# Performance work log

Measured on AMD Instinct MI355X. Metric: run time of the kernel, lower is better.

## Reference

```python
import jax, jax.numpy as jnp
import numpy as np

D_MODEL = 256
NHEAD = 8
NLAYERS = 4
DFF = 1024
PATCH = 8
INPUT = 32
C = 2
DATA_DIM = C * PATCH * PATCH  # 128
P = (INPUT // PATCH) ** 2     # 16
NEG = -1.0e6                  # _neg_large_for_dtype(float32)
EPS = 1e-5


def _ln(x, w, b):
    m = x.mean(-1, keepdims=True)
    v = ((x - m) ** 2).mean(-1, keepdims=True)
    return (x - m) / jnp.sqrt(v + EPS) * w + b


def _forward(img_baseline, acq_dts_float, nan_token, pad_embed, emb_w, emb_b, spatial_pos,
             t_w1, t_b1, t_w2, t_b2, t_w3, t_b3,
             in_proj_w, in_proj_b, out_proj_w, out_proj_b,
             lin1_w, lin1_b, lin2_w, lin2_b, norm1_w, norm1_b, norm2_w, norm2_b,
             mean_w1, mean_b1, mean_w2, mean_b2, lv_w1, lv_b1, lv_w2, lv_b2):
    B, T, Cc, Hh, Ww = img_baseline.shape
    p = PATCH
    gh, gw = Hh // p, Ww // p
    L = T * P
    frame_pad = jnp.all(img_baseline == -9999.0, axis=(2, 3, 4))  # (B,T)
    nan_pix = jnp.isnan(img_baseline)
    token = jnp.clip(nan_token, -10.0, 10.0).reshape(1, 1, Cc, 1, 1)
    x = jnp.clip(jnp.where(nan_pix, token, img_baseline), -10.0, 10.0)

    def patchify(a):  # b t c (h ph)(w pw) -> b t (h w) (c ph pw)
        return a.reshape(B, T, Cc, gh, p, gw, p).transpose(0, 1, 3, 5, 2, 4, 6).reshape(B, T, P, Cc * p * p)

    xp = patchify(x)
    seq_nan = patchify(nan_pix).all(-1).reshape(B, L)
    seq_pad = jnp.broadcast_to(frame_pad[:, :, None], (B, T, P)).reshape(B, L)

    # temporal MLP embedding
    t_in = jnp.where(jnp.isnan(acq_dts_float), 0.0, acq_dts_float)[..., None]  # (B,T,1)
    h = jax.nn.relu(t_in @ t_w1.T + t_b1)
    h = jax.nn.relu(h @ t_w2.T + t_b2)
    temb = h @ t_w3.T + t_b3  # (B,T,D)

    z = xp @ emb_w.T + emb_b + spatial_pos + temb[:, :, None, :]  # (B,T,P,D)
    z = z.reshape(B, L, D_MODEL)
    z = jnp.where(seq_pad[..., None], pad_embed, z)  # masked_scatter of pad_embed

    # additive attention mask: rows with NaN/pad patches are fully masked except diagonal
    masked_rows = seq_nan | seq_pad
    mask = jnp.broadcast_to(jnp.where(masked_rows[:, :, None], NEG, 0.0), (B, L, L))
    eye = jnp.eye(L, dtype=bool)
    mask = jnp.where(eye[None, :, :] & masked_rows[:, :, None], 0.0, mask)
    # key_padding_mask merged additively on key columns
    mask = mask + jnp.where(seq_pad[:, None, :], NEG, 0.0)
    mask = mask[:, None, :, :]  # (B,1,L,L), shared across heads

    dh = D_MODEL // NHEAD
    scale = 1.0 / np.sqrt(dh).astype(np.float32)
    for l in range(NLAYERS):
        qkv = z @ in_proj_w[l].T + in_proj_b[l]
        q, k, v = jnp.split(qkv, 3, axis=-1)
        q = q.reshape(B, L, NHEAD, dh).transpose(0, 2, 1, 3)
        k = k.reshape(B, L, NHEAD, dh).transpose(0, 2, 1, 3)
        v = v.reshape(B, L, NHEAD, dh).transpose(0, 2, 1, 3)
        scores = jnp.einsum('bhqd,bhkd->bhqk', q, k) * scale + mask
        attn = jax.nn.softmax(scores, axis=-1)
        o = jnp.einsum('bhqk,bhkd->bhqd', attn, v).transpose(0, 2, 1, 3).reshape(B, L, D_MODEL)
        o = o @ out_proj_w[l].T + out_proj_b[l]
        z = _ln(z + o, norm1_w[l], norm1_b[l])
        ff = jax.nn.relu(z @ lin1_w[l].T + lin1_b[l]) @ lin2_w[l].T + lin2_b[l]
        z = _ln(z + ff, norm2_w[l], norm2_b[l])

    mean = jnp.clip(jax.nn.relu(z @ mean_w1.T + mean_b1) @ mean_w2.T + mean_b2, -10.0, 10.0)
    logvar = jnp.clip(jax.nn.relu(z @ lv_w1.T + lv_b1) @ lv_w2.T + lv_b2, -10.0, 5.0)

    def unpatch(a):  # b t (h w)(c ph pw) -> b t c (h ph)(w pw)
        return a.reshape(B, T, gh, gw, Cc, p, p).transpose(0, 1, 4, 2, 5, 3, 6).reshape(B, T, Cc, Hh, Ww)

    mean = unpatch(mean.reshape(B, T, P, DATA_DIM))
    logvar = unpatch(logvar.reshape(B, T, P, DATA_DIM))
    return mean[:, -1], logvar[:, -1]


def setup_inputs() -> dict:
    key = jax.random.key(0)
    ks = iter(jax.random.split(key, 48))

    def rn(shape, scale=0.02):
        return jax.random.normal(next(ks), shape, dtype=jnp.float32) * scale

    B, T = 4, 64
    z = lambda s: jnp.zeros(s, jnp.float32)
    return {
        'img_baseline': jax.random.normal(next(ks), (B, T, C, INPUT, INPUT), dtype=jnp.float32),
        'acq_dts_float': jax.random.uniform(next(ks), (B, T), dtype=jnp.float32) * 3000.0,
        'nan_token': rn((C,)),
        'pad_embed': rn((1, 1, D_MODEL)),
        'emb_w': rn((D_MODEL, DATA_DIM)),
        'emb_b': z((D_MODEL,)),
        'spatial_pos': rn((1, 1, P, D_MODEL)),
        't_w1': rn((64, 1)), 't_b1': z((64,)),
        't_w2': rn((128, 64)), 't_b2': z((128,)),
        't_w3': rn((D_MODEL, 128)), 't_b3': z((D_MODEL,)),
        'in_proj_w': rn((NLAYERS, 3 * D_MODEL, D_MODEL)),
        'in_proj_b': z((NLAYERS, 3 * D_MODEL)),
        'out_proj_w': rn((NLAYERS, D_MODEL, D_MODEL)),
        'out_proj_b': z((NLAYERS, D_MODEL)),
        'lin1_w': rn((NLAYERS, DFF, D_MODEL)), 'lin1_b': z((NLAYERS, DFF)),
        'lin2_w': rn((NLAYERS, D_MODEL, DFF)), 'lin2_b': z((NLAYERS, D_MODEL)),
        'norm1_w': jnp.ones((NLAYERS, D_MODEL), jnp.float32), 'norm1_b': z((NLAYERS, D_MODEL)),
        'norm2_w': jnp.ones((NLAYERS, D_MODEL), jnp.float32), 'norm2_b': z((NLAYERS, D_MODEL)),
        'mean_w1': rn((DFF, D_MODEL)), 'mean_b1': z((DFF,)),
        'mean_w2': rn((DATA_DIM, DFF)), 'mean_b2': z((DATA_DIM,)),
        'lv_w1': rn((DFF, D_MODEL)), 'lv_b1': z((DFF,)),
        'lv_w2': rn((DATA_DIM, DFF)), 'lv_b2': z((DATA_DIM,)),
    }


def reference(img_baseline, acq_dts_float, nan_token, pad_embed, emb_w, emb_b, spatial_pos,
              t_w1, t_b1, t_w2, t_b2, t_w3, t_b3,
              in_proj_w, in_proj_b, out_proj_w, out_proj_b,
              lin1_w, lin1_b, lin2_w, lin2_b, norm1_w, norm1_b, norm2_w, norm2_b,
              mean_w1, mean_b1, mean_w2, mean_b2, lv_w1, lv_b1, lv_w2, lv_b2):
    return _forward(img_baseline, acq_dts_float, nan_token, pad_embed, emb_w, emb_b, spatial_pos,
                    t_w1, t_b1, t_w2, t_b2, t_w3, t_b3,
                    in_proj_w, in_proj_b, out_proj_w, out_proj_b,
                    lin1_w, lin1_b, lin2_w, lin2_b, norm1_w, norm1_b, norm2_w, norm2_b,
                    mean_w1, mean_b1, mean_w2, mean_b2, lv_w1, lv_b1, lv_w2, lv_b2)
```

## Files before the change

### kernel.cpp

```cpp
#include <hip/hip_runtime.h>
#include <hip/hip_bf16.h>

#define D_MODEL 256
#define NHEAD 8
#define DH 32
#define NLAYERS 4
#define DFF 1024
#define CC 2
#define DATA_DIM 128
#define PP 16
#define TT 64
#define BB 4
#define LL 1024
#define NEGV -1000000.0f

typedef __bf16 bf16_t;
typedef __bf16 bf16x8 __attribute__((ext_vector_type(8)));
typedef __bf16 bf16x4 __attribute__((ext_vector_type(4)));
typedef float v4f __attribute__((ext_vector_type(4)));

__device__ __forceinline__ bool my_isnan(float v) {
    unsigned u = __float_as_uint(v);
    return (u & 0x7fffffffu) > 0x7f800000u;
}

__device__ __forceinline__ void gld16(bf16_t* l, const bf16_t* g) {
    __builtin_amdgcn_global_load_lds(
        (const __attribute__((address_space(1))) void*)g,
        (__attribute__((address_space(3))) void*)l, 16, 0, 0);
}

__global__ void f2b_all_kernel(const float* __restrict__ s0, bf16_t* __restrict__ d0, int n0,
                               const float* __restrict__ s1, bf16_t* __restrict__ d1, int n1,
                               const float* __restrict__ s2, bf16_t* __restrict__ d2, int n2,
                               const float* __restrict__ s3, bf16_t* __restrict__ d3, int n3,
                               const float* __restrict__ s4, bf16_t* __restrict__ d4, int n4,
                               const float* __restrict__ s5, bf16_t* __restrict__ d5, int n5,
                               const float* __restrict__ s6, bf16_t* __restrict__ d6, int n6,
                               const float* __restrict__ s7, bf16_t* __restrict__ d7, int n7,
                               const float* __restrict__ s8, bf16_t* __restrict__ d8, int n8) {
    int i = (blockIdx.x * 256 + threadIdx.x) * 4;
    const float* s;
    bf16_t* d;
    if (i < n0) { s = s0; d = d0; }
    else if ((i -= n0) < n1) { s = s1; d = d1; }
    else if ((i -= n1) < n2) { s = s2; d = d2; }
    else if ((i -= n2) < n3) { s = s3; d = d3; }
    else if ((i -= n3) < n4) { s = s4; d = d4; }
    else if ((i -= n4) < n5) { s = s5; d = d5; }
    else if ((i -= n5) < n6) { s = s6; d = d6; }
    else if ((i -= n6) < n7) { s = s7; d = d7; }
    else if ((i -= n7) < n8) { s = s8; d = d8; }
    else return;
    float4 v = *(const float4*)(s + i);
    bf16x4 o = {(bf16_t)v.x, (bf16_t)v.y, (bf16_t)v.z, (bf16_t)v.w};
    *(bf16x4*)(d + i) = o;
}

__global__ void prep_frame_kernel(const float* __restrict__ img,
                                  const float* __restrict__ acq,
                                  const float* __restrict__ t_w1, const float* __restrict__ t_b1,
                                  const float* __restrict__ t_w2, const float* __restrict__ t_b2,
                                  const float* __restrict__ t_w3, const float* __restrict__ t_b3,
                                  float* __restrict__ temb, int* __restrict__ framepad) {
    int f = blockIdx.x;
    int tid = threadIdx.x;
    __shared__ float h1[64];
    __shared__ float h2[128];
    __shared__ int sAll;
    if (tid == 0) sAll = 1;
    __syncthreads();
    const float* fr = img + (size_t)f * (CC * 32 * 32);
    bool allpad = true;
    #pragma unroll
    for (int i = 0; i < 8; ++i) {
        float v = fr[tid + i * 256];
        allpad = allpad && (v == -9999.0f);
    }
    if (!allpad) sAll = 0;
    __syncthreads();
    if (tid == 0) framepad[f] = sAll;

    float t_in = acq[f];
    if (my_isnan(t_in)) t_in = 0.0f;
    if (tid < 64) h1[tid] = fmaxf(t_w1[tid] * t_in + t_b1[tid], 0.0f);
    __syncthreads();
    if (tid < 128) {
        float a = t_b2[tid];
        #pragma unroll 8
        for (int j = 0; j < 64; ++j) a += t_w2[tid * 64 + j] * h1[j];
        h2[tid] = fmaxf(a, 0.0f);
    }
    __syncthreads();
    {
        float a = t_b3[tid];
        #pragma unroll 8
        for (int j = 0; j < 128; ++j) a += t_w3[tid * 128 + j] * h2[j];
        temb[(size_t)f * D_MODEL + tid] = a;
    }
}

__global__ __launch_bounds__(256) void patchify_kernel(
    const float* __restrict__ img, const float* __restrict__ nan_token,
    const int* __restrict__ framepad,
    bf16_t* __restrict__ xpb, int* __restrict__ masked_rows,
    float* __restrict__ kmaskf) {
    int tid = threadIdx.x;
    int token = blockIdx.x * 2 + (tid >> 7);
    int dd = tid & 127;
    int l = token & 1023, b = token >> 10;
    int t = l >> 4, p = l & 15;
    int c = dd >> 6, pr = (dd >> 3) & 7, pc = dd & 7;
    int hh = (p >> 2) * 8 + pr, ww = (p & 3) * 8 + pc;
    float v = img[(((size_t)(b * TT + t) * CC + c) * 32 + hh) * 32 + ww];
    bool nanp = my_isnan(v);
    if (nanp) v = fminf(fmaxf(nan_token[c], -10.0f), 10.0f);
    v = fminf(fmaxf(v, -10.0f), 10.0f);
    xpb[(size_t)token * DATA_DIM + dd] = (bf16_t)v;

    __shared__ int wAll[4];
    unsigned long long bal = __ballot(nanp);
    if ((tid & 63) == 0) wAll[tid >> 6] = (bal == 0xFFFFFFFFFFFFFFFFull) ? 1 : 0;
    __syncthreads();
    if (tid < 2) {
        int tk = blockIdx.x * 2 + tid;
        int allnan = wAll[tid * 2] & wAll[tid * 2 + 1];
        int fp = framepad[tk >> 4];
        masked_rows[tk] = allnan | fp;
        kmaskf[tk] = fp ? NEGV : 0.0f;
    }
}

__global__ __launch_bounds__(256) void embed_gemm(
    const bf16_t* __restrict__ X, const bf16_t* __restrict__ W,
    const float* __restrict__ emb_b, const float* __restrict__ spatial,
    const float* __restrict__ temb, const float* __restrict__ pad_embed,
    const int* __restrict__ framepad,
    bf16_t* __restrict__ zb) {
    __shared__ __align__(16) bf16_t Xs[128 * 32];
    __shared__ __align__(16) bf16_t Ws[64 * 32];
    int tid = threadIdx.x;
    int wave = tid >> 6, lane = tid & 63;
    int quad = lane >> 4, l16 = lane & 15;
    int m0 = blockIdx.y * 128, n0 = blockIdx.x * 64;
    const int K = DATA_DIM, N = D_MODEL;

    v4f acc[2][4];
    #pragma unroll
    for (int i = 0; i < 2; ++i)
        #pragma unroll
        for (int j = 0; j < 4; ++j) acc[i][j] = (v4f){0.f, 0.f, 0.f, 0.f};

    int sr = tid >> 2, ss = tid & 3;
    for (int k0 = 0; k0 < K; k0 += 32) {
        gld16(Xs + tid * 8, X + (size_t)(m0 + sr) * K + k0 + ss * 8);
        gld16(Xs + 2048 + tid * 8, X + (size_t)(m0 + 64 + sr) * K + k0 + ss * 8);
        gld16(Ws + tid * 8, W + (size_t)(n0 + sr) * K + k0 + ss * 8);
        __syncthreads();
        bf16x8 af0 = *(const bf16x8*)(Xs + (wave * 32 + l16) * 32 + quad * 8);
        bf16x8 af1 = *(const bf16x8*)(Xs + (wave * 32 + 16 + l16) * 32 + quad * 8);
        #pragma unroll
        for (int nt = 0; nt < 4; ++nt) {
            bf16x8 bfr = *(const bf16x8*)(Ws + (nt * 16 + l16) * 32 + quad * 8);
            acc[0][nt] = __builtin_amdgcn_mfma_f32_16x16x32_bf16(af0, bfr, acc[0][nt], 0, 0, 0);
            acc[1][nt] = __builtin_amdgcn_mfma_f32_16x16x32_bf16(af1, bfr, acc[1][nt], 0, 0, 0);
        }
        __syncthreads();
    }

    #pragma unroll
    for (int mt = 0; mt < 2; ++mt)
        #pragma unroll
        for (int nt = 0; nt < 4; ++nt) {
            int col = n0 + nt * 16 + l16;
            #pragma unroll
            for (int reg = 0; reg < 4; ++reg) {
                int row = m0 + wave * 32 + mt * 16 + quad * 4 + reg;
                int frame = row >> 4, p = row & 15;
                float v;
                if (framepad[frame]) {
                    v = pad_embed[col];
                } else {
                    v = acc[mt][nt][reg] + emb_b[col] + spatial[p * N + col]
                      + temb[(size_t)frame * N + col];
                }
                zb[(size_t)row * N + col] = (bf16_t)v;
            }
        }
}

template <int MODE, int RELU>
__global__ __launch_bounds__(256) void gemm_mfma(
    const bf16_t* __restrict__ X, const bf16_t* __restrict__ W,
    const float* __restrict__ bias, bf16_t* __restrict__ Y,
    bf16_t* __restrict__ Vt, int M, int N, int K) {
    __shared__ __align__(16) bf16_t Xs[2][128 * 32];
    __shared__ __align__(16) bf16_t Ws[2][64 * 32];
    int tid = threadIdx.x;
    int wave = tid >> 6, lane = tid & 63;
    int quad = lane >> 4, l16 = lane & 15;
    int m0 = blockIdx.y * 128, n0 = blockIdx.x * 64;

    v4f acc[2][4];
    #pragma unroll
    for (int i = 0; i < 2; ++i)
        #pragma unroll
        for (int j = 0; j < 4; ++j) acc[i][j] = (v4f){0.f, 0.f, 0.f, 0.f};

    int sr = tid >> 2, ss = tid & 3;
    for (int k0 = 0; k0 < K; k0 += 64) {
        #pragma unroll
        for (int half = 0; half < 2; ++half) {
            int kh = k0 + half * 32;
            gld16(Xs[half] + tid * 8, X + (size_t)(m0 + sr) * K + kh + ss * 8);
            gld16(Xs[half] + 2048 + tid * 8, X + (size_t)(m0 + 64 + sr) * K + kh + ss * 8);
            gld16(Ws[half] + tid * 8, W + (size_t)(n0 + sr) * K + kh + ss * 8);
        }
        __syncthreads();
        #pragma unroll
        for (int half = 0; half < 2; ++half) {
            bf16x8 af0 = *(const bf16x8*)(Xs[half] + (wave * 32 + l16) * 32 + quad * 8);
            bf16x8 af1 = *(const bf16x8*)(Xs[half] + (wave * 32 + 16 + l16) * 32 + quad * 8);
            #pragma unroll
            for (int nt = 0; nt < 4; ++nt) {
                bf16x8 bfr = *(const bf16x8*)(Ws[half] + (nt * 16 + l16) * 32 + quad * 8);
                acc[0][nt] = __builtin_amdgcn_mfma_f32_16x16x32_bf16(af0, bfr, acc[0][nt], 0, 0, 0);
                acc[1][nt] = __builtin_amdgcn_mfma_f32_16x16x32_bf16(af1, bfr, acc[1][nt], 0, 0, 0);
            }
        }
        __syncthreads();
    }

    if constexpr (MODE == 1) {
        #pragma unroll
        for (int mt = 0; mt < 2; ++mt)
            #pragma unroll
            for (int nt = 0; nt < 4; ++nt) {
                int col = n0 + nt * 16 + l16;
                float bv = bias[col];
                #pragma unroll
                for (int reg = 0; reg < 4; ++reg) {
                    int row = m0 + wave * 32 + mt * 16 + quad * 4 + reg;
                    float v = acc[mt][nt][reg] + bv;
                    if (RELU) v = fmaxf(v, 0.0f);
                    Y[(size_t)row * N + col] = (bf16_t)v;
                }
            }
    } else {
        if (n0 < 512) {
            #pragma unroll
            for (int mt = 0; mt < 2; ++mt)
                #pragma unroll
                for (int nt = 0; nt < 4; ++nt) {
                    int col = n0 + nt * 16 + l16;
                    float bv = bias[col];
                    #pragma unroll
                    for (int reg = 0; reg < 4; ++reg) {
                        int row = m0 + wave * 32 + mt * 16 + quad * 4 + reg;
                        float v = acc[mt][nt][reg] + bv;
                        Y[(size_t)row * 768 + col] = (bf16_t)v;
                    }
                }
        } else {
            __shared__ __align__(16) bf16_t VT[64 * 136];
            #pragma unroll
            for (int mt = 0; mt < 2; ++mt)
                #pragma unroll
                for (int nt = 0; nt < 4; ++nt) {
                    int cl = nt * 16 + l16;
                    float bv = bias[n0 + cl];
                    #pragma unroll
                    for (int reg = 0; reg < 4; ++reg) {
                        int rl = wave * 32 + mt * 16 + quad * 4 + reg;
                        VT[cl * 136 + rl] = (bf16_t)(acc[mt][nt][reg] + bv);
                    }
                }
            __syncthreads();
            int b = m0 >> 10, l0m = m0 & 1023;
            int cl = tid >> 2;
            int rbase = (tid & 3) * 8;
            int cg = n0 + cl - 512;
            int h = cg >> 5, d = cg & 31;
            bf16_t* dst = Vt + (((size_t)(b * NHEAD + h)) * DH + d) * LL + l0m;
            #pragma unroll
            for (int u = 0; u < 4; ++u)
                *(uint4*)(dst + rbase + u * 32) = *(const uint4*)(VT + cl * 136 + rbase + u * 32);
        }
    }
}

__global__ __launch_bounds__(256) void gemm_small(
    const bf16_t* __restrict__ X, const bf16_t* __restrict__ W,
    const float* __restrict__ bias, const bf16_t* __restrict__ Zres,
    bf16_t* __restrict__ Y, int M, int N, int K) {
    __shared__ __align__(16) bf16_t Xs[2][64 * 32];
    __shared__ __align__(16) bf16_t Ws[2][64 * 32];
    int tid = threadIdx.x;
    int wave = tid >> 6, lane = tid & 63;
    int quad = lane >> 4, l16 = lane & 15;
    int m0 = blockIdx.y * 64, n0 = blockIdx.x * 64;

    v4f acc[4];
    #pragma unroll
    for (int j = 0; j < 4; ++j) acc[j] = (v4f){0.f, 0.f, 0.f, 0.f};

    int sr = tid >> 2, ss = tid & 3;
    for (int k0 = 0; k0 < K; k0 += 64) {
        #pragma unroll
        for (int half = 0; half < 2; ++half) {
            int kh = k0 + half * 32;
            gld16(Xs[half] + tid * 8, X + (size_t)(m0 + sr) * K + kh + ss * 8);
            gld16(Ws[half] + tid * 8, W + (size_t)(n0 + sr) * K + kh + ss * 8);
        }
        __syncthreads();
        #pragma unroll
        for (int half = 0; half < 2; ++half) {
            bf16x8 af = *(const bf16x8*)(Xs[half] + (wave * 16 + l16) * 32 + quad * 8);
            #pragma unroll
            for (int nt = 0; nt < 4; ++nt) {
                bf16x8 bfr = *(const bf16x8*)(Ws[half] + (nt * 16 + l16) * 32 + quad * 8);
                acc[nt] = __builtin_amdgcn_mfma_f32_16x16x32_bf16(af, bfr, acc[nt], 0, 0, 0);
            }
        }
        __syncthreads();
    }

    #pragma unroll
    for (int nt = 0; nt < 4; ++nt) {
        int col = n0 + nt * 16 + l16;
        float bv = bias[col];
        #pragma unroll
        for (int reg = 0; reg < 4; ++reg) {
            int row = m0 + wave * 16 + quad * 4 + reg;
            float r = acc[nt][reg] + bv + (float)Zres[(size_t)row * N + col];
            Y[(size_t)row * N + col] = (bf16_t)r;
        }
    }
}

__global__ __launch_bounds__(256) void attn_mfma(
    const bf16_t* __restrict__ qkvb, const bf16_t* __restrict__ Vt,
    const int* __restrict__ masked_rows, const float* __restrict__ kmaskf,
    bf16_t* __restrict__ Ob) {
    __shared__ __align__(16) bf16_t Ks[2][128 * 40];
    __shared__ __align__(16) bf16_t Vs[2][32 * 136];
    __shared__ __align__(16) float  Kms[2][128];
    __shared__ __align__(16) bf16_t Ps[4][16 * 136];

    int tid = threadIdx.x;
    int wave = tid >> 6, lane = tid & 63;
    int quad = lane >> 4, l16 = lane & 15;
    int bid = blockIdx.x;
    int h = bid & 7, b = (bid >> 3) & 3, qt = bid >> 5;
    int q0 = qt * 64 + wave * 16;
    const float scale = 0.17677669529663687f;

    bf16x8 qf = *(const bf16x8*)(qkvb + ((size_t)(b * LL) + q0 + l16) * 768 + h * DH + quad * 8);

    int mq = masked_rows[b * LL + q0 + l16];
    int qg = q0 + l16;

    float lrun = 0.0f;
    v4f oacc[2];
    oacc[0] = (v4f){0.f, 0.f, 0.f, 0.f};
    oacc[1] = (v4f){0.f, 0.f, 0.f, 0.f};

    int kr = tid >> 1, kh = (tid & 1) * 16;
    int vd = tid >> 3, vs0 = (tid & 7) * 8;
    const bf16_t* Kbase = qkvb + (size_t)(b * LL) * 768 + 256 + h * DH;
    const bf16_t* Vbase = Vt + (((size_t)(b * NHEAD + h)) * DH) * LL;
    const float* kmbase = kmaskf + b * LL;

    uint4 ka, kb, va, vb;
    float kmg;
    #define LOADC(c)                                                            \
        do {                                                                    \
            int _k0 = (c) * 128;                                                \
            ka = *(const uint4*)(Kbase + (size_t)(_k0 + kr) * 768 + kh);        \
            kb = *(const uint4*)(Kbase + (size_t)(_k0 + kr) * 768 + kh + 8);    \
            va = *(const uint4*)(Vbase + (size_t)vd * LL + _k0 + vs0);          \
            vb = *(const uint4*)(Vbase + (size_t)vd * LL + _k0 + 64 + vs0);     \
            kmg = (tid < 128) ? kmbase[_k0 + tid] : 0.0f;                       \
        } while (0)
    #define WRITEBUF(buf)                                                       \
        do {                                                                    \
            *(uint4*)(Ks[(buf)] + kr * 40 + kh) = ka;                           \
            *(uint4*)(Ks[(buf)] + kr * 40 + kh + 8) = kb;                       \
            *(uint4*)(Vs[(buf)] + vd * 136 + vs0) = va;                         \
            *(uint4*)(Vs[(buf)] + vd * 136 + 64 + vs0) = vb;                    \
            if (tid < 128) Kms[(buf)][tid] = kmg;                               \
        } while (0)

    LOADC(0);
    WRITEBUF(0);
    LOADC(1);

    bf16_t* Pw = Ps[wave];
    for (int c = 0; c < 8; ++c) {
        __syncthreads();
        int cur = c & 1;
        if (c + 1 < 8) WRITEBUF(cur ^ 1);
        if (c + 2 < 8) LOADC(c + 2);

        int k0 = c * 128;
        const bf16_t* Kc = Ks[cur];
        const bf16_t* Vc = Vs[cur];
        const float* kmc = Kms[cur];

        v4f sf[8];
        #pragma unroll
        for (int nt = 0; nt < 8; ++nt) {
            bf16x8 kf = *(const bf16x8*)(Kc + (nt * 16 + l16) * 40 + quad * 8);
            v4f zf = (v4f){0.f, 0.f, 0.f, 0.f};
            sf[nt] = __builtin_amdgcn_mfma_f32_16x16x32_bf16(kf, qf, zf, 0, 0, 0);
        }

        #pragma unroll
        for (int nt = 0; nt < 8; ++nt) {
            int kbase_nt = k0 + nt * 16 + quad * 4;
            float4 kmv = *(const float4*)(kmc + nt * 16 + quad * 4);
            float pv[4];
            #pragma unroll
            for (int reg = 0; reg < 4; ++reg) {
                float km = (reg == 0) ? kmv.x : (reg == 1) ? kmv.y : (reg == 2) ? kmv.z : kmv.w;
                float v = sf[nt][reg] * scale + km;
                if (mq && (qg != kbase_nt + reg)) v += NEGV;
                float p = __expf(v);
                lrun += p;
                pv[reg] = p;
            }
            bf16x4 pp = {(bf16_t)pv[0], (bf16_t)pv[1], (bf16_t)pv[2], (bf16_t)pv[3]};
            *(bf16x4*)(Pw + l16 * 136 + nt * 16 + quad * 4) = pp;
        }

        #pragma unroll
        for (int kt = 0; kt < 4; ++kt) {
            bf16x8 pf = *(const bf16x8*)(Pw + l16 * 136 + kt * 32 + quad * 8);
            #pragma unroll
            for (int nt2 = 0; nt2 < 2; ++nt2) {
                bf16x8 vf = *(const bf16x8*)(Vc + (nt2 * 16 + l16) * 136 + kt * 32 + quad * 8);
                oacc[nt2] = __builtin_amdgcn_mfma_f32_16x16x32_bf16(pf, vf, oacc[nt2], 0, 0, 0);
            }
        }
    }
    #undef LOADC
    #undef WRITEBUF

    lrun += __shfl_xor(lrun, 16);
    lrun += __shfl_xor(lrun, 32);
    float lq[4];
    #pragma unroll
    for (int reg = 0; reg < 4; ++reg) lq[reg] = __shfl(lrun, quad * 4 + reg);

    #pragma unroll
    for (int nt2 = 0; nt2 < 2; ++nt2)
        #pragma unroll
        for (int reg = 0; reg < 4; ++reg) {
            size_t row = (size_t)(b * LL) + q0 + quad * 4 + reg;
            Ob[row * 256 + h * DH + nt2 * 16 + l16] = (bf16_t)(oacc[nt2][reg] / lq[reg]);
        }
}

__global__ __launch_bounds__(256) void ln_kernel(
    const bf16_t* __restrict__ tmps, const float* __restrict__ w,
    const float* __restrict__ b, bf16_t* __restrict__ zb) {
    int wave = threadIdx.x >> 6, lane = threadIdx.x & 63;
    int row = blockIdx.x * 4 + wave;
    bf16x4 xb = *(const bf16x4*)(tmps + (size_t)row * D_MODEL + lane * 4);
    float x0 = (float)xb[0], x1 = (float)xb[1], x2 = (float)xb[2], x3 = (float)xb[3];
    float s = x0 + x1 + x2 + x3;
    #pragma unroll
    for (int off = 32; off > 0; off >>= 1) s += __shfl_xor(s, off);
    float mean = s * (1.0f / D_MODEL);
    float dx0 = x0 - mean, dx1 = x1 - mean, dx2 = x2 - mean, dx3 = x3 - mean;
    float sq = dx0 * dx0 + dx1 * dx1 + dx2 * dx2 + dx3 * dx3;
    #pragma unroll
    for (int off = 32; off > 0; off >>= 1) sq += __shfl_xor(sq, off);
    float inv = 1.0f / sqrtf(sq * (1.0f / D_MODEL) + 1e-5f);
    float4 wv = ((const float4*)w)[lane];
    float4 bv = ((const float4*)b)[lane];
    bf16x4 rb = {(bf16_t)(dx0 * inv * wv.x + bv.x),
                 (bf16_t)(dx1 * inv * wv.y + bv.y),
                 (bf16_t)(dx2 * inv * wv.z + bv.z),
                 (bf16_t)(dx3 * inv * wv.w + bv.w)};
    *(bf16x4*)(zb + (size_t)row * D_MODEL + lane * 4) = rb;
}

__global__ __launch_bounds__(256) void head_h_kernel(
    const bf16_t* __restrict__ zb, const bf16_t* __restrict__ W1b,
    const float* __restrict__ mean_b1, const float* __restrict__ lv_b1,
    bf16_t* __restrict__ hb) {
    __shared__ __align__(16) bf16_t Xs[64 * 32];
    __shared__ __align__(16) bf16_t Ws[64 * 32];
    int tid = threadIdx.x;
    int wave = tid >> 6, lane = tid & 63;
    int quad = lane >> 4, l16 = lane & 15;
    int head = blockIdx.y;
    int n0 = blockIdx.x * 64;
    const bf16_t* W1h = W1b + (size_t)head * DFF * D_MODEL;
    const float* B1f = head ? lv_b1 : mean_b1;
    bf16_t* hbh = hb + (size_t)head * 64 * DFF;

    v4f acc[4];
    #pragma unroll
    for (int j = 0; j < 4; ++j) acc[j] = (v4f){0.f, 0.f, 0.f, 0.f};

    int sr = tid >> 2, ss = tid & 3;
    int gb = sr >> 4, gp = sr & 15;
    const bf16_t* xrow = zb + ((size_t)(gb * LL + (TT - 1) * PP + gp)) * D_MODEL;
    for (int k0 = 0; k0 < D_MODEL; k0 += 32) {
        gld16(Xs + tid * 8, xrow + k0 + ss * 8);
        gld16(Ws + tid * 8, W1h + (size_t)(n0 + sr) * D_MODEL + k0 + ss * 8);
        __syncthreads();
        bf16x8 af = *(const bf16x8*)(Xs + (wave * 16 + l16) * 32 + quad * 8);
        #pragma unroll
        for (int nt = 0; nt < 4; ++nt) {
            bf16x8 bfr = *(const bf16x8*)(Ws + (nt * 16 + l16) * 32 + quad * 8);
            acc[nt] = __builtin_amdgcn_mfma_f32_16x16x32_bf16(af, bfr, acc[nt], 0, 0, 0);
        }
        __syncthreads();
    }

    #pragma unroll
    for (int nt = 0; nt < 4; ++nt) {
        int col = n0 + nt * 16 + l16;
        float bv = B1f[col];
        #pragma unroll
        for (int reg = 0; reg < 4; ++reg) {
            int row = wave * 16 + quad * 4 + reg;
            hbh[(size_t)row * DFF + col] = (bf16_t)fmaxf(acc[nt][reg] + bv, 0.0f);
        }
    }
}

__global__ __launch_bounds__(256) void head_out_kernel(
    const bf16_t* __restrict__ hb, const bf16_t* __restrict__ W2b,
    const float* __restrict__ mean_b2, const float* __restrict__ lv_b2,
    float* __restrict__ out) {
    __shared__ __align__(16) bf16_t hrow[DFF];
    int tid = threadIdx.x;
    int bid = blockIdx.x;
    int head = bid >> 7, rr = (bid >> 1) & 63, half = bid & 1;
    int b = rr >> 4, p = rr & 15;

    if (tid < 128)
        *(uint4*)(hrow + tid * 8) =
            *(const uint4*)(hb + ((size_t)head * 64 + rr) * DFF + tid * 8);
    __syncthreads();

    int ol = tid >> 2, quarter = tid & 3;
    int o = half * 64 + ol;
    const bf16_t* wrow = W2b + ((size_t)head * DATA_DIM + o) * DFF + quarter * 256;
    const bf16_t* hseg = hrow + quarter * 256;
    float acc = 0.0f;
    #pragma unroll 8
    for (int j = 0; j < 32; ++j) {
        bf16x8 w = *(const bf16x8*)(wrow + j * 8);
        bf16x8 hv = *(const bf16x8*)(hseg + j * 8);
        #pragma unroll
        for (int e = 0; e < 8; ++e) acc += (float)w[e] * (float)hv[e];
    }
    acc += __shfl_xor(acc, 1);
    acc += __shfl_xor(acc, 2);
    if (quarter == 0) {
        const float* B2 = head ? lv_b2 : mean_b2;
        float hi = head ? 5.0f : 10.0f;
        float v = fminf(fmaxf(acc + B2[o], -10.0f), hi);
        int c = o >> 6;
        int pr = (o >> 3) & 7, pc = o & 7;
        int hh = (p >> 2) * 8 + pr, ww = (p & 3) * 8 + pc;
        out[(size_t)head * 8192 + ((size_t)(b * CC + c)) * 1024 + hh * 32 + ww] = v;
    }
}

extern "C" void kernel_launch(void* const* d_in, const int* in_sizes, int n_in,
                              void* d_out, int out_size, void* d_ws, size_t ws_size,
                              hipStream_t stream) {
    const float* img        = (const float*)d_in[0];
    const float* acq        = (const float*)d_in[1];
    const float* nan_token  = (const float*)d_in[2];
    const float* pad_embed  = (const float*)d_in[3];
    const float* emb_w      = (const float*)d_in[4];
    const float* emb_b      = (const float*)d_in[5];
    const float* spatial    = (const float*)d_in[6];
    const float* t_w1       = (const float*)d_in[7];
    const float* t_b1       = (const float*)d_in[8];
    const float* t_w2       = (const float*)d_in[9];
    const float* t_b2       = (const float*)d_in[10];
    const float* t_w3       = (const float*)d_in[11];
    const float* t_b3       = (const float*)d_in[12];
    const float* in_proj_w  = (const float*)d_in[13];
    const float* in_proj_b  = (const float*)d_in[14];
    const float* out_proj_w = (const float*)d_in[15];
    const float* out_proj_b = (const float*)d_in[16];
    const float* lin1_w     = (const float*)d_in[17];
    const float* lin1_b     = (const float*)d_in[18];
    const float* lin2_w     = (const float*)d_in[19];
    const float* lin2_b     = (const float*)d_in[20];
    const float* norm1_w    = (const float*)d_in[21];
    const float* norm1_b    = (const float*)d_in[22];
    const float* norm2_w    = (const float*)d_in[23];
    const float* norm2_b    = (const float*)d_in[24];
    const float* mean_w1    = (const float*)d_in[25];
    const float* mean_b1    = (const float*)d_in[26];
    const float* mean_w2    = (const float*)d_in[27];
    const float* mean_b2    = (const float*)d_in[28];
    const float* lv_w1      = (const float*)d_in[29];
    const float* lv_b1      = (const float*)d_in[30];
    const float* lv_w2      = (const float*)d_in[31];
    const float* lv_b2      = (const float*)d_in[32];

    const int M = BB * LL;

    char* wsb = (char*)d_ws;
    float* temb    = (float*)wsb;                    wsb += (size_t)BB * TT * D_MODEL * 4;
    float* kmaskf  = (float*)wsb;                    wsb += M * 4;
    int* framepad  = (int*)wsb;                      wsb += BB * TT * 4;
    int* masked    = (int*)wsb;                      wsb += M * 4;
    wsb = (char*)(((uintptr_t)wsb + 255) & ~(uintptr_t)255);
    bf16_t* zb     = (bf16_t*)wsb;                   wsb += (size_t)M * D_MODEL * 2;
    bf16_t* tmps   = (bf16_t*)wsb;                   wsb += (size_t)M * D_MODEL * 2;
    bf16_t* xpb    = (bf16_t*)wsb;                   wsb += (size_t)M * DATA_DIM * 2;
    bf16_t* qkvb   = (bf16_t*)wsb;                   wsb += (size_t)M * 768 * 2;
    bf16_t* VtG    = (bf16_t*)wsb;                   wsb += (size_t)M * D_MODEL * 2;
    bf16_t* attnb  = (bf16_t*)wsb;                   wsb += (size_t)M * D_MODEL * 2;
    bf16_t* ff1b   = (bf16_t*)wsb;                   wsb += (size_t)M * DFF * 2;
    bf16_t* inb    = (bf16_t*)wsb;                   wsb += (size_t)NLAYERS * 768 * D_MODEL * 2;
    bf16_t* outb   = (bf16_t*)wsb;                   wsb += (size_t)NLAYERS * D_MODEL * D_MODEL * 2;
    bf16_t* l1b    = (bf16_t*)wsb;                   wsb += (size_t)NLAYERS * DFF * D_MODEL * 2;
    bf16_t* l2b    = (bf16_t*)wsb;                   wsb += (size_t)NLAYERS * D_MODEL * DFF * 2;
    bf16_t* embwb  = (bf16_t*)wsb;                   wsb += (size_t)D_MODEL * DATA_DIM * 2;
    bf16_t* w1b    = (bf16_t*)wsb;                   wsb += (size_t)2 * DFF * D_MODEL * 2;
    bf16_t* w2b    = (bf16_t*)wsb;                   wsb += (size_t)2 * DATA_DIM * DFF * 2;
    bf16_t* hb     = (bf16_t*)wsb;                   wsb += (size_t)2 * 64 * DFF * 2;

    float* outF = (float*)d_out;

    {
        int n1 = NLAYERS * 768 * D_MODEL;
        int n2 = NLAYERS * D_MODEL * D_MODEL;
        int n3 = NLAYERS * DFF * D_MODEL;
        int n4 = NLAYERS * D_MODEL * DFF;
        int n5 = D_MODEL * DATA_DIM;
        int n6 = DFF * D_MODEL;
        int n7 = DFF * D_MODEL;
        int n8 = DATA_DIM * DFF;
        int n9 = DATA_DIM * DFF;
        int tot = n1 + n2 + n3 + n4 + n5 + n6 + n7 + n8 + n9;
        f2b_all_kernel<<<(tot / 4 + 255) / 256, 256, 0, stream>>>(
            in_proj_w, inb, n1, out_proj_w, outb, n2, lin1_w, l1b, n3,
            lin2_w, l2b, n4, emb_w, embwb, n5,
            mean_w1, w1b, n6, lv_w1, w1b + (size_t)DFF * D_MODEL, n7,
            mean_w2, w2b, n8, lv_w2, w2b + (size_t)DATA_DIM * DFF, n9);
    }

    prep_frame_kernel<<<BB * TT, 256, 0, stream>>>(img, acq, t_w1, t_b1, t_w2, t_b2,
                                                   t_w3, t_b3, temb, framepad);
    patchify_kernel<<<M / 2, 256, 0, stream>>>(img, nan_token, framepad, xpb, masked, kmaskf);
    embed_gemm<<<dim3(D_MODEL / 64, M / 128), 256, 0, stream>>>(
        xpb, embwb, emb_b, spatial, temb, pad_embed, framepad, zb);

    for (int l = 0; l < NLAYERS; ++l) {
        gemm_mfma<2, 0><<<dim3(768 / 64, M / 128), 256, 0, stream>>>(
            zb, inb + (size_t)l * 768 * D_MODEL, in_proj_b + (size_t)l * 768,
            qkvb, VtG, M, 768, D_MODEL);
        attn_mfma<<<BB * NHEAD * (LL / 64), 256, 0, stream>>>(qkvb, VtG, masked, kmaskf, attnb);
        gemm_small<<<dim3(D_MODEL / 64, M / 64), 256, 0, stream>>>(
            attnb, outb + (size_t)l * D_MODEL * D_MODEL, out_proj_b + (size_t)l * D_MODEL,
            zb, tmps, M, D_MODEL, D_MODEL);
        ln_kernel<<<M / 4, 256, 0, stream>>>(tmps, norm1_w + l * D_MODEL,
                                             norm1_b + l * D_MODEL, zb);
        gemm_mfma<1, 1><<<dim3(DFF / 64, M / 128), 256, 0, stream>>>(
            zb, l1b + (size_t)l * DFF * D_MODEL, lin1_b + (size_t)l * DFF,
            ff1b, nullptr, M, DFF, D_MODEL);
        gemm_small<<<dim3(D_MODEL / 64, M / 64), 256, 0, stream>>>(
            ff1b, l2b + (size_t)l * D_MODEL * DFF, lin2_b + (size_t)l * D_MODEL,
            zb, tmps, M, D_MODEL, DFF);
        ln_kernel<<<M / 4, 256, 0, stream>>>(tmps, norm2_w + l * D_MODEL,
                                             norm2_b + l * D_MODEL, zb);
    }

    head_h_kernel<<<dim3(DFF / 64, 2), 256, 0, stream>>>(zb, w1b, mean_b1, lv_b1, hb);
    head_out_kernel<<<256, 256, 0, stream>>>(hb, w2b, mean_b2, lv_b2, outF);
}
```

Measured before the change: 398.6 us.

## Double-buffer GEMM k-tiles with XOR-swizzled 64-wide LDS layout across kernels

All MFMA GEMM kernels (embed, qkv/ffn, residual, head) now stage 64-wide K tiles into ping-pong LDS buffers. The next tile's global loads are issued before computing on the current one, which removes one barrier per step and overlaps memory with MFMA work. An XOR swizzle on the 16-byte column groups is meant to avoid LDS bank conflicts when fragments are read from 128-byte rows. The V-transpose scratch reuses the X staging buffer, which keeps LDS usage down but raises it versus before for the other kernels and may reduce occupancy.

```diff
diff --git a/kernel.cpp b/kernel.cpp
--- a/kernel.cpp
+++ b/kernel.cpp
@@ -137,8 +137,8 @@
     const float* __restrict__ temb, const float* __restrict__ pad_embed,
     const int* __restrict__ framepad,
     bf16_t* __restrict__ zb) {
-    __shared__ __align__(16) bf16_t Xs[128 * 32];
-    __shared__ __align__(16) bf16_t Ws[64 * 32];
+    __shared__ __align__(16) bf16_t Xs[2][128 * 64];
+    __shared__ __align__(16) bf16_t Ws[2][64 * 64];
     int tid = threadIdx.x;
     int wave = tid >> 6, lane = tid & 63;
     int quad = lane >> 4, l16 = lane & 15;
@@ -151,22 +151,48 @@
         #pragma unroll
         for (int j = 0; j < 4; ++j) acc[i][j] = (v4f){0.f, 0.f, 0.f, 0.f};
 
-    int sr = tid >> 2, ss = tid & 3;
-    for (int k0 = 0; k0 < K; k0 += 32) {
-        gld16(Xs + tid * 8, X + (size_t)(m0 + sr) * K + k0 + ss * 8);
-        gld16(Xs + 2048 + tid * 8, X + (size_t)(m0 + 64 + sr) * K + k0 + ss * 8);
-        gld16(Ws + tid * 8, W + (size_t)(n0 + sr) * K + k0 + ss * 8);
+    int sr = tid >> 3, ss = tid & 7;
+    int gc = (ss ^ (sr & 7)) * 8;
+
+#define ESTAGE(bufi, k0)                                                          \
+    do {                                                                          \
+        _Pragma("unroll")                                                         \
+        for (int p = 0; p < 4; ++p) {                                             \
+            int r = sr + p * 32;                                                  \
+            gld16(Xs[bufi] + r * 64 + ss * 8, X + (size_t)(m0 + r) * K + (k0) + gc); \
+        }                                                                         \
+        _Pragma("unroll")                                                         \
+        for (int p = 0; p < 2; ++p) {                                             \
+            int r = sr + p * 32;                                                  \
+            gld16(Ws[bufi] + r * 64 + ss * 8, W + (size_t)(n0 + r) * K + (k0) + gc); \
+        }                                                                         \
+    } while (0)
+
+    ESTAGE(0, 0);
+    __syncthreads();
+    const int T = K / 64;
+    int swl = l16 & 7;
+    for (int t = 0; t < T; ++t) {
+        int buf = t & 1;
+        if (t + 1 < T) ESTAGE(buf ^ 1, (t + 1) * 64);
+        const bf16_t* Xc = Xs[buf];
+        const bf16_t* Wc = Ws[buf];
+        int ra = wave * 32 + l16;
+        #pragma unroll
+        for (int h = 0; h < 2; ++h) {
+            int g8 = ((h * 4 + quad) ^ swl) * 8;
+            bf16x8 af0 = *(const bf16x8*)(Xc + ra * 64 + g8);
+            bf16x8 af1 = *(const bf16x8*)(Xc + (ra + 16) * 64 + g8);
+            #pragma unroll
+            for (int nt = 0; nt < 4; ++nt) {
+                bf16x8 bfr = *(const bf16x8*)(Wc + (nt * 16 + l16) * 64 + g8);
+                acc[0][nt] = __builtin_amdgcn_mfma_f32_16x16x32_bf16(af0, bfr, acc[0][nt], 0, 0, 0);
+                acc[1][nt] = __builtin_amdgcn_mfma_f32_16x16x32_bf16(af1, bfr, acc[1][nt], 0, 0, 0);
+            }
+        }
         __syncthreads();
-        bf16x8 af0 = *(const bf16x8*)(Xs + (wave * 32 + l16) * 32 + quad * 8);
-        bf16x8 af1 = *(const bf16x8*)(Xs + (wave * 32 + 16 + l16) * 32 + quad * 8);
-        #pragma unroll
-        for (int nt = 0; nt < 4; ++nt) {
-            bf16x8 bfr = *(const bf16x8*)(Ws + (nt * 16 + l16) * 32 + quad * 8);
-            acc[0][nt] = __builtin_amdgcn_mfma_f32_16x16x32_bf16(af0, bfr, acc[0][nt], 0, 0, 0);
-            acc[1][nt] = __builtin_amdgcn_mfma_f32_16x16x32_bf16(af1, bfr, acc[1][nt], 0, 0, 0);
-        }
-        __syncthreads();
-    }
+    }
+#undef ESTAGE
 
     #pragma unroll
     for (int mt = 0; mt < 2; ++mt)
@@ -194,8 +220,8 @@
     const bf16_t* __restrict__ X, const bf16_t* __restrict__ W,
     const float* __restrict__ bias, bf16_t* __restrict__ Y,
     bf16_t* __restrict__ Vt, int M, int N, int K) {
-    __shared__ __align__(16) bf16_t Xs[2][128 * 32];
-    __shared__ __align__(16) bf16_t Ws[2][64 * 32];
+    __shared__ __align__(16) bf16_t Xs[2][128 * 64];
+    __shared__ __align__(16) bf16_t Ws[2][64 * 64];
     int tid = threadIdx.x;
     int wave = tid >> 6, lane = tid & 63;
     int quad = lane >> 4, l16 = lane & 15;
@@ -207,29 +233,48 @@
         #pragma unroll
         for (int j = 0; j < 4; ++j) acc[i][j] = (v4f){0.f, 0.f, 0.f, 0.f};
 
-    int sr = tid >> 2, ss = tid & 3;
-    for (int k0 = 0; k0 < K; k0 += 64) {
-        #pragma unroll
-        for (int half = 0; half < 2; ++half) {
-            int kh = k0 + half * 32;
-            gld16(Xs[half] + tid * 8, X + (size_t)(m0 + sr) * K + kh + ss * 8);
-            gld16(Xs[half] + 2048 + tid * 8, X + (size_t)(m0 + 64 + sr) * K + kh + ss * 8);
-            gld16(Ws[half] + tid * 8, W + (size_t)(n0 + sr) * K + kh + ss * 8);
-        }
-        __syncthreads();
-        #pragma unroll
-        for (int half = 0; half < 2; ++half) {
-            bf16x8 af0 = *(const bf16x8*)(Xs[half] + (wave * 32 + l16) * 32 + quad * 8);
-            bf16x8 af1 = *(const bf16x8*)(Xs[half] + (wave * 32 + 16 + l16) * 32 + quad * 8);
+    int sr = tid >> 3, ss = tid & 7;
+    int gc = (ss ^ (sr & 7)) * 8;
+
+#define GSTAGE(bufi, k0)                                                          \
+    do {                                                                          \
+        _Pragma("unroll")                                                         \
+        for (int p = 0; p < 4; ++p) {                                             \
+            int r = sr + p * 32;                                                  \
+            gld16(Xs[bufi] + r * 64 + ss * 8, X + (size_t)(m0 + r) * K + (k0) + gc); \
+        }                                                                         \
+        _Pragma("unroll")                                                         \
+        for (int p = 0; p < 2; ++p) {                                             \
+            int r = sr + p * 32;                                                  \
+            gld16(Ws[bufi] + r * 64 + ss * 8, W + (size_t)(n0 + r) * K + (k0) + gc); \
+        }                                                                         \
+    } while (0)
+
+    GSTAGE(0, 0);
+    __syncthreads();
+    const int T = K >> 6;
+    int swl = l16 & 7;
+    for (int t = 0; t < T; ++t) {
+        int buf = t & 1;
+        if (t + 1 < T) GSTAGE(buf ^ 1, (t + 1) * 64);
+        const bf16_t* Xc = Xs[buf];
+        const bf16_t* Wc = Ws[buf];
+        int ra = wave * 32 + l16;
+        #pragma unroll
+        for (int h = 0; h < 2; ++h) {
+            int g8 = ((h * 4 + quad) ^ swl) * 8;
+            bf16x8 af0 = *(const bf16x8*)(Xc + ra * 64 + g8);
+            bf16x8 af1 = *(const bf16x8*)(Xc + (ra + 16) * 64 + g8);
             #pragma unroll
             for (int nt = 0; nt < 4; ++nt) {
-                bf16x8 bfr = *(const bf16x8*)(Ws[half] + (nt * 16 + l16) * 32 + quad * 8);
+                bf16x8 bfr = *(const bf16x8*)(Wc + (nt * 16 + l16) * 64 + g8);
                 acc[0][nt] = __builtin_amdgcn_mfma_f32_16x16x32_bf16(af0, bfr, acc[0][nt], 0, 0, 0);
                 acc[1][nt] = __builtin_amdgcn_mfma_f32_16x16x32_bf16(af1, bfr, acc[1][nt], 0, 0, 0);
             }
         }
         __syncthreads();
     }
+#undef GSTAGE
 
     if constexpr (MODE == 1) {
         #pragma unroll
@@ -262,7 +307,7 @@
                     }
                 }
         } else {
-            __shared__ __align__(16) bf16_t VT[64 * 136];
+            bf16_t* VT = &Xs[0][0];
             #pragma unroll
             for (int mt = 0; mt < 2; ++mt)
                 #pragma unroll
@@ -293,8 +338,8 @@
     const bf16_t* __restrict__ X, const bf16_t* __restrict__ W,
     const float* __restrict__ bias, const bf16_t* __restrict__ Zres,
     bf16_t* __restrict__ Y, int M, int N, int K) {
-    __shared__ __align__(16) bf16_t Xs[2][64 * 32];
-    __shared__ __align__(16) bf16_t Ws[2][64 * 32];
+    __shared__ __align__(16) bf16_t Xs[2][64 * 64];
+    __shared__ __align__(16) bf16_t Ws[2][64 * 64];
     int tid = threadIdx.x;
     int wave = tid >> 6, lane = tid & 63;
     int quad = lane >> 4, l16 = lane & 15;
@@ -304,26 +349,42 @@
     #pragma unroll
     for (int j = 0; j < 4; ++j) acc[j] = (v4f){0.f, 0.f, 0.f, 0.f};
 
-    int sr = tid >> 2, ss = tid & 3;
-    for (int k0 = 0; k0 < K; k0 += 64) {
-        #pragma unroll
-        for (int half = 0; half < 2; ++half) {
-            int kh = k0 + half * 32;
-            gld16(Xs[half] + tid * 8, X + (size_t)(m0 + sr) * K + kh + ss * 8);
-            gld16(Ws[half] + tid * 8, W + (size_t)(n0 + sr) * K + kh + ss * 8);
-        }
-        __syncthreads();
-        #pragma unroll
-        for (int half = 0; half < 2; ++half) {
-            bf16x8 af = *(const bf16x8*)(Xs[half] + (wave * 16 + l16) * 32 + quad * 8);
+    int sr = tid >> 3, ss = tid & 7;
+    int gc = (ss ^ (sr & 7)) * 8;
+
+#define SSTAGE(bufi, k0)                                                          \
+    do {                                                                          \
+        _Pragma("unroll")                                                         \
+        for (int p = 0; p < 2; ++p) {                                             \
+            int r = sr + p * 32;                                                  \
+            gld16(Xs[bufi] + r * 64 + ss * 8, X + (size_t)(m0 + r) * K + (k0) + gc); \
+            gld16(Ws[bufi] + r * 64 + ss * 8, W + (size_t)(n0 + r) * K + (k0) + gc); \
+        }                                                                         \
+    } while (0)
+
+    SSTAGE(0, 0);
+    __syncthreads();
+    const int T = K >> 6;
+    int swl = l16 & 7;
+    for (int t = 0; t < T; ++t) {
+        int buf = t & 1;
+        if (t + 1 < T) SSTAGE(buf ^ 1, (t + 1) * 64);
+        const bf16_t* Xc = Xs[buf];
+        const bf16_t* Wc = Ws[buf];
+        int ra = wave * 16 + l16;
+        #pragma unroll
+        for (int h = 0; h < 2; ++h) {
+            int g8 = ((h * 4 + quad) ^ swl) * 8;
+            bf16x8 af = *(const bf16x8*)(Xc + ra * 64 + g8);
             #pragma unroll
             for (int nt = 0; nt < 4; ++nt) {
-                bf16x8 bfr = *(const bf16x8*)(Ws[half] + (nt * 16 + l16) * 32 + quad * 8);
+                bf16x8 bfr = *(const bf16x8*)(Wc + (nt * 16 + l16) * 64 + g8);
                 acc[nt] = __builtin_amdgcn_mfma_f32_16x16x32_bf16(af, bfr, acc[nt], 0, 0, 0);
             }
         }
         __syncthreads();
     }
+#undef SSTAGE
 
     #pragma unroll
     for (int nt = 0; nt < 4; ++nt) {
@@ -490,8 +551,8 @@
     const bf16_t* __restrict__ zb, const bf16_t* __restrict__ W1b,
     const float* __restrict__ mean_b1, const float* __restrict__ lv_b1,
     bf16_t* __restrict__ hb) {
-    __shared__ __align__(16) bf16_t Xs[64 * 32];
-    __shared__ __align__(16) bf16_t Ws[64 * 32];
+    __shared__ __align__(16) bf16_t Xs[2][64 * 64];
+    __shared__ __align__(16) bf16_t Ws[2][64 * 64];
     int tid = threadIdx.x;
     int wave = tid >> 6, lane = tid & 63;
     int quad = lane >> 4, l16 = lane & 15;
@@ -505,21 +566,43 @@
     #pragma unroll
     for (int j = 0; j < 4; ++j) acc[j] = (v4f){0.f, 0.f, 0.f, 0.f};
 
-    int sr = tid >> 2, ss = tid & 3;
-    int gb = sr >> 4, gp = sr & 15;
-    const bf16_t* xrow = zb + ((size_t)(gb * LL + (TT - 1) * PP + gp)) * D_MODEL;
-    for (int k0 = 0; k0 < D_MODEL; k0 += 32) {
-        gld16(Xs + tid * 8, xrow + k0 + ss * 8);
-        gld16(Ws + tid * 8, W1h + (size_t)(n0 + sr) * D_MODEL + k0 + ss * 8);
+    int sr = tid >> 3, ss = tid & 7;
+    int gc = (ss ^ (sr & 7)) * 8;
+
+#define HSTAGE(bufi, k0)                                                          \
+    do {                                                                          \
+        _Pragma("unroll")                                                         \
+        for (int p = 0; p < 2; ++p) {                                             \
+            int r = sr + p * 32;                                                  \
+            const bf16_t* xr = zb + (size_t)((r >> 4) * LL + (TT - 1) * PP + (r & 15)) * D_MODEL; \
+            gld16(Xs[bufi] + r * 64 + ss * 8, xr + (k0) + gc);                    \
+            gld16(Ws[bufi] + r * 64 + ss * 8, W1h + (size_t)(n0 + r) * D_MODEL + (k0) + gc); \
+        }                                                                         \
+    } while (0)
+
+    HSTAGE(0, 0);
+    __syncthreads();
+    const int T = D_MODEL / 64;
+    int swl = l16 & 7;
+    for (int t = 0; t < T; ++t) {
+        int buf = t & 1;
+        if (t + 1 < T) HSTAGE(buf ^ 1, (t + 1) * 64);
+        const bf16_t* Xc = Xs[buf];
+        const bf16_t* Wc = Ws[buf];
+        int ra = wave * 16 + l16;
+        #pragma unroll
+        for (int h = 0; h < 2; ++h) {
+            int g8 = ((h * 4 + quad) ^ swl) * 8;
+            bf16x8 af = *(const bf16x8*)(Xc + ra * 64 + g8);
+            #pragma unroll
+            for (int nt = 0; nt < 4; ++nt) {
+                bf16x8 bfr = *(const bf16x8*)(Wc + (nt * 16 + l16) * 64 + g8);
+                acc[nt] = __builtin_amdgcn_mfma_f32_16x16x32_bf16(af, bfr, acc[nt], 0, 0, 0);
+            }
+        }
         __syncthreads();
-        bf16x8 af = *(const bf16x8*)(Xs + (wave * 16 + l16) * 32 + quad * 8);
-        #pragma unroll
-        for (int nt = 0; nt < 4; ++nt) {
-            bf16x8 bfr = *(const bf16x8*)(Ws + (nt * 16 + l16) * 32 + quad * 8);
-            acc[nt] = __builtin_amdgcn_mfma_f32_16x16x32_bf16(af, bfr, acc[nt], 0, 0, 0);
-        }
-        __syncthreads();
-    }
+    }
+#undef HSTAGE
 
     #pragma unroll
     for (int nt = 0; nt < 4; ++nt) {
```

Result: no change. 396.1 us (-0.6%).
